# Kernel optimization log

Measured on AMD Instinct MI355X. Metric: run time of the kernel, lower is better.

Reference implementation:

```python
import jax, jax.numpy as jnp
import numpy as np

DIM = 256
NUM_ATOMS = 1024
SPARSITY = 8
BETA = 0.25
EPS = 1e-10


def setup_inputs() -> dict:
    key = jax.random.key(0)
    k1, k2, k3, k4 = jax.random.split(key, 4)
    z_e = jax.random.normal(k1, (32, DIM, 32, 32), dtype=jnp.float32)
    dict_w = jax.random.normal(k2, (NUM_ATOMS, DIM), dtype=jnp.float32)
    rep_w = jax.random.normal(k3, (NUM_ATOMS, DIM), dtype=jnp.float32) * (1.0 / np.sqrt(DIM))
    rep_b = jnp.zeros((NUM_ATOMS,), dtype=jnp.float32)
    return {"z_e": z_e, "dict_w": dict_w, "rep_w": rep_w, "rep_b": rep_b}


def reference(z_e, dict_w, rep_w, rep_b):
    # NCHW -> NHWC, flatten to [N, D]
    ze = jnp.transpose(z_e, (0, 2, 3, 1))
    ze_shape = ze.shape
    flat = ze.reshape(-1, DIM)  # [N, D]
    n = flat.shape[0]

    # representation: Linear + softmax over atoms
    rep = jax.nn.softmax(flat @ rep_w.T + rep_b, axis=1)  # [N, K]

    # squared distances to dictionary atoms
    dists = (jnp.sum(flat ** 2, axis=1, keepdims=True)
             + jnp.sum(dict_w ** 2, axis=1)
             - 2.0 * (flat @ dict_w.T))  # [N, K]

    # top-L smallest distances
    _, idx = jax.lax.top_k(-dists, SPARSITY)  # [N, L]

    # one-hot scatter of selected atoms
    encodings = jnp.zeros((n, NUM_ATOMS), dtype=flat.dtype)
    encodings = encodings.at[jnp.arange(n)[:, None], idx].set(1.0)

    rep_sparse = encodings * rep / SPARSITY  # [N, K]
    z_dl = (rep_sparse @ dict_w).reshape(ze_shape)  # [B, H, W, D]

    e_latent_loss = jnp.mean((jax.lax.stop_gradient(z_dl) - ze) ** 2)
    loss = BETA * e_latent_loss

    # straight-through estimator
    z_st = ze + jax.lax.stop_gradient(z_dl - ze)

    avg_probs = jnp.mean(encodings, axis=0)
    avg_probs = avg_probs / jnp.sum(avg_probs)
    perplexity = jnp.exp(-jnp.sum(avg_probs * jnp.log(avg_probs + EPS)))

    return loss, jnp.transpose(z_st, (0, 3, 1, 2)), perplexity, rep_sparse
```

## Files before the change

kernel.cpp:

```cpp
#include <hip/hip_runtime.h>
#include <hip/hip_bf16.h>
#include <stdint.h>

#define NROWS   32768
#define DIMD    256
#define NATOMS  1024

typedef short  bf16x8 __attribute__((ext_vector_type(8)));
typedef float  f32x4  __attribute__((ext_vector_type(4)));

__device__ __forceinline__ unsigned short bf16rne(float f) {
    unsigned u = __float_as_uint(f);
    u = u + 0x7FFFu + ((u >> 16) & 1u);
    return (unsigned short)(u >> 16);
}

__global__ __launch_bounds__(256) void vq_bprep(
    const float* __restrict__ rep_w, const float* __restrict__ dict_w,
    unsigned short* __restrict__ Bs, float* __restrict__ dnorm,
    int* __restrict__ counts)
{
    const int tid = threadIdx.x;
    if (blockIdx.x == 0) {
        for (int i = tid; i < NATOMS; i += 256) counts[i] = 0;
    }
    const int atom = blockIdx.x * 32 + (tid >> 3);
    const int kc = tid & 7;
    float ss = 0.f;
#pragma unroll
    for (int m = 0; m < 2; ++m) {
        const float* src = (m ? dict_w : rep_w) + (size_t)atom * DIMD + kc * 32;
        unsigned short* dst = Bs + (size_t)m * 262144 + (size_t)kc * 32768 + atom * 32;
#pragma unroll
        for (int q = 0; q < 8; ++q) {
            float4 v = *(const float4*)&src[q * 4];
            float fv[4] = {v.x, v.y, v.z, v.w};
            unsigned short a0[4];
#pragma unroll
            for (int e = 0; e < 4; ++e) {
                if (m) ss = fmaf(fv[e], fv[e], ss);
                a0[e] = bf16rne(fv[e]);
            }
            *(ushort4*)&dst[q * 4] = make_ushort4(a0[0], a0[1], a0[2], a0[3]);
        }
    }
    ss += __shfl_down(ss, 4, 8);
    ss += __shfl_down(ss, 2, 8);
    ss += __shfl_down(ss, 1, 8);
    if (kc == 0) dnorm[atom] = ss;
}

__device__ __forceinline__ void insk(unsigned u, unsigned (&kd)[8]) {
#pragma unroll
    for (int j = 7; j >= 1; --j)
        kd[j] = min(max(u, kd[j - 1]), kd[j]);
    kd[0] = min(u, kd[0]);
}

__device__ __forceinline__ void wave_merge_k(int lane, unsigned (&kd)[8], float& se) {
#pragma unroll
    for (int half = 32; half >= 16; half >>= 1) {
        const int src = (lane + half) & 63;
        unsigned ko[8];
#pragma unroll
        for (int j = 0; j < 8; ++j) ko[j] = (unsigned)__shfl((int)kd[j], src, 64);
        const float so = __shfl(se, src, 64);
        if (lane < half) {
            se += so;
#pragma unroll
            for (int t = 0; t < 8; ++t) insk(ko[t], kd);
        }
    }
}

__global__ __launch_bounds__(256, 3) void vq_main(
    const float* __restrict__ z_e, const unsigned short* __restrict__ Bs,
    const float* __restrict__ rep_b, const float* __restrict__ dnorm,
    int* __restrict__ idx_out, float* __restrict__ fsum_out)
{
    __shared__ __align__(16) float rbS[1024];
    __shared__ __align__(16) float dnS[1024];
    __shared__ unsigned mKu[3][32][8];
    __shared__ float mS[3][32];
    __shared__ unsigned fK[32][8];
    __shared__ float fSum[32];

    const int tid = threadIdx.x;
    const int lane = tid & 63, w = tid >> 6;
    const int c = lane & 15, lg = lane >> 4;
    const int row0 = blockIdx.x * 32;
    const int bb = row0 >> 10, hw0 = row0 & 1023;

    for (int i = tid; i < 1024; i += 256) { rbS[i] = rep_b[i]; dnS[i] = dnorm[i]; }

    const char* pL = (const char*)Bs;
    const char* pD = (const char*)Bs + 524288;
    const int abase = w << 8;

    bf16x8 bL[8], bD[8];
    {
        const int off = ((abase + c) << 6) + (lg << 4);
#pragma unroll
        for (int kc = 0; kc < 8; ++kc) {
            bL[kc] = *(const bf16x8*)(pL + ((size_t)kc << 16) + off);
            bD[kc] = *(const bf16x8*)(pD + ((size_t)kc << 16) + off);
        }
    }

    bf16x8 A0[8], A1[8];
    {
        const float* zb = z_e + (size_t)bb * 262144 + hw0 + c;
#pragma unroll
        for (int kc = 0; kc < 8; ++kc) {
            float f0[8], f1[8];
#pragma unroll
            for (int e = 0; e < 8; ++e) {
                const float* p = zb + (size_t)(kc * 32 + lg * 8 + e) * 1024;
                f0[e] = p[0];
                f1[e] = p[16];
            }
#pragma unroll
            for (int e = 0; e < 8; ++e) {
                A0[kc][e] = (short)bf16rne(f0[e]);
                A1[kc][e] = (short)bf16rne(f1[e]);
            }
        }
    }
    __syncthreads();

    unsigned kd0[8], kd1[8];
    float se0 = 0.f, se1 = 0.f;
#pragma unroll
    for (int j = 0; j < 8; ++j) { kd0[j] = 0xFFFFFFFFu; kd1[j] = 0xFFFFFFFFu; }

    for (int it = 0; it < 16; ++it) {
        const int tb = abase + (it << 4) + (lg << 2);
        const f32x4 rbv = *(const f32x4*)&rbS[tb];
        const f32x4 dnv = *(const f32x4*)&dnS[tb];

        f32x4 aL0 = {0.f,0.f,0.f,0.f}, aD0 = {0.f,0.f,0.f,0.f};
        f32x4 aL1 = {0.f,0.f,0.f,0.f}, aD1 = {0.f,0.f,0.f,0.f};
#pragma unroll
        for (int kc = 0; kc < 8; ++kc) {
            aL0 = __builtin_amdgcn_mfma_f32_16x16x32_bf16(bL[kc], A0[kc], aL0, 0, 0, 0);
            aD0 = __builtin_amdgcn_mfma_f32_16x16x32_bf16(bD[kc], A0[kc], aD0, 0, 0, 0);
            aL1 = __builtin_amdgcn_mfma_f32_16x16x32_bf16(bL[kc], A1[kc], aL1, 0, 0, 0);
            aD1 = __builtin_amdgcn_mfma_f32_16x16x32_bf16(bD[kc], A1[kc], aD1, 0, 0, 0);
        }

        if (it < 15) {
            const int off = ((abase + (it + 1) * 16 + c) << 6) + (lg << 4);
#pragma unroll
            for (int kc = 0; kc < 8; ++kc) {
                bL[kc] = *(const bf16x8*)(pL + ((size_t)kc << 16) + off);
                bD[kc] = *(const bf16x8*)(pD + ((size_t)kc << 16) + off);
            }
        }

#pragma unroll
        for (int q = 0; q < 4; ++q) {
            const unsigned atom = (unsigned)(tb + q);
            se0 += __expf(aL0[q] + rbv[q]);
            se1 += __expf(aL1[q] + rbv[q]);
            unsigned u0 = __float_as_uint(dnv[q] - 2.0f * aD0[q]);
            u0 ^= ((unsigned)((int)u0 >> 31) | 0x80000000u);
            unsigned u1 = __float_as_uint(dnv[q] - 2.0f * aD1[q]);
            u1 ^= ((unsigned)((int)u1 >> 31) | 0x80000000u);
            insk((u0 & ~1023u) | atom, kd0);
            insk((u1 & ~1023u) | atom, kd1);
        }
    }

    wave_merge_k(lane, kd0, se0);
    wave_merge_k(lane, kd1, se1);

    if (w >= 1 && lane < 16) {
#pragma unroll
        for (int j = 0; j < 8; ++j) {
            mKu[w - 1][c][j] = kd0[j];
            mKu[w - 1][16 + c][j] = kd1[j];
        }
        mS[w - 1][c] = se0;
        mS[w - 1][16 + c] = se1;
    }
    __syncthreads();

    if (w == 0 && lane < 16) {
        for (int p = 0; p < 3; ++p)
#pragma unroll
            for (int t = 0; t < 8; ++t) {
                insk(mKu[p][c][t], kd0);
                insk(mKu[p][16 + c][t], kd1);
            }
        se0 += mS[0][c] + mS[1][c] + mS[2][c];
        se1 += mS[0][16 + c] + mS[1][16 + c] + mS[2][16 + c];
#pragma unroll
        for (int j = 0; j < 8; ++j) { fK[c][j] = kd0[j]; fK[16 + c][j] = kd1[j]; }
        fSum[c] = se0;
        fSum[16 + c] = se1;
    }
    __syncthreads();

    {
        const int j = tid >> 5, rr = tid & 31;
        idx_out[(row0 + rr) * 8 + j] = (int)(fK[rr][j] & 1023u);
    }
    if (tid < 32) fsum_out[row0 + tid] = fSum[tid];
}

__global__ __launch_bounds__(256, 4) void vq_recon(
    const float* __restrict__ z_e, const float* __restrict__ dict_w,
    const float* __restrict__ rep_w, const float* __restrict__ rep_b,
    const int* __restrict__ idx_in, const float* __restrict__ fsum_in,
    float* __restrict__ rep_sparse, float* __restrict__ z_st,
    float* __restrict__ partials, int* __restrict__ counts)
{
    __shared__ __align__(16) float zL[32][260];
    __shared__ int   iS[256];
    __shared__ float wS[256];
    __shared__ float fS[32];
    __shared__ float red[256];

    const int tid = threadIdx.x;
    const int row0 = blockIdx.x * 32;
    const int bb = row0 >> 10, hw0 = row0 & 1023;
    const float* zb = z_e + (size_t)bb * 262144 + hw0;

    {
        float4 z4 = {0.f, 0.f, 0.f, 0.f};
        float4* rp4 = (float4*)rep_sparse + (size_t)row0 * (NATOMS / 4) + tid;
        for (int r = 0; r < 32; ++r)
            rp4[(size_t)r * (NATOMS / 4)] = z4;
    }

    iS[tid] = idx_in[row0 * 8 + tid];
    if (tid < 32) fS[tid] = fsum_in[row0 + tid];
    {
        const int m = tid & 31, dg = tid >> 5;
        for (int it = 0; it < 32; ++it) {
            const int d = it * 8 + dg;
            zL[m][d] = zb[(size_t)d * 1024 + m];
        }
    }
    __syncthreads();

    {
        const int j = tid >> 5, rr = tid & 31;
        const int idx = iS[rr * 8 + j];
        const float* rw = rep_w + (size_t)idx * DIMD;
        float acc = 0.f;
        for (int k = 0; k < DIMD; k += 4) {
            const float4 rv = *(const float4*)&rw[k];
            const f32x4 zv = *(const f32x4*)&zL[rr][k];
            acc = fmaf(zv[0], rv.x, acc);
            acc = fmaf(zv[1], rv.y, acc);
            acc = fmaf(zv[2], rv.z, acc);
            acc = fmaf(zv[3], rv.w, acc);
        }
        wS[rr * 8 + j] = __expf(acc + rep_b[idx]) * 0.125f / fS[rr];
    }
    __syncthreads();

    {
        const int j = tid >> 5, rr = tid & 31;
        rep_sparse[(size_t)(row0 + rr) * NATOMS + iS[rr * 8 + j]] = wS[rr * 8 + j];
    }

    float sacc = 0.f;
    for (int r = 0; r < 32; ++r) {
        float acc = 0.f;
#pragma unroll
        for (int j = 0; j < 8; ++j) {
            const int ix = iS[r * 8 + j];
            const float wv = wS[r * 8 + j];
            acc = fmaf(wv, dict_w[(size_t)ix * DIMD + tid], acc);
        }
        const float ze = zL[r][tid];
        const float diff = acc - ze;
        sacc = fmaf(diff, diff, sacc);
        zL[r][tid] = acc;
    }
    __syncthreads();

    {
        float* ob = z_st + (size_t)bb * 262144 + hw0;
        const int m = tid & 31, dg = tid >> 5;
        for (int it = 0; it < 32; ++it) {
            const int d = it * 8 + dg;
            ob[(size_t)d * 1024 + m] = zL[m][d];
        }
    }

    red[tid] = sacc;
    __syncthreads();
    for (int s = 128; s > 0; s >>= 1) {
        if (tid < s) red[tid] += red[tid + s];
        __syncthreads();
    }
    if (tid == 0) partials[blockIdx.x] = red[0];

    __syncthreads();
    int* hS = (int*)zL;
    for (int i = tid; i < 1024; i += 256) hS[i] = 0;
    __syncthreads();
    atomicAdd(&hS[iS[tid]], 1);
    __syncthreads();
    for (int i = tid; i < 1024; i += 256)
        if (hS[i]) atomicAdd(&counts[i], hS[i]);
}

__global__ void vq_final(const float* __restrict__ partials,
                         const int* __restrict__ counts,
                         float* __restrict__ out_loss, float* __restrict__ out_perp)
{
    __shared__ double dred[256];
    __shared__ float fred[256];
    const int tid = threadIdx.x;
    double s = 0.0;
    for (int i = tid; i < 1024; i += 256) s += (double)partials[i];
    dred[tid] = s;
    __syncthreads();
    for (int st = 128; st > 0; st >>= 1) {
        if (tid < st) dred[tid] += dred[tid + st];
        __syncthreads();
    }
    float ps = 0.f;
    for (int i = tid; i < NATOMS; i += 256) {
        const float p = (float)counts[i] * (1.0f / 262144.0f);
        ps += p * logf(p + 1e-10f);
    }
    fred[tid] = ps;
    __syncthreads();
    for (int st = 128; st > 0; st >>= 1) {
        if (tid < st) fred[tid] += fred[tid + st];
        __syncthreads();
    }
    if (tid == 0) {
        *out_loss = 0.25f * (float)(dred[0] / 8388608.0);
        *out_perp = expf(-fred[0]);
    }
}

extern "C" void kernel_launch(void* const* d_in, const int* in_sizes, int n_in,
                              void* d_out, int out_size, void* d_ws, size_t ws_size,
                              hipStream_t stream) {
    const float* z_e    = (const float*)d_in[0];
    const float* dict_w = (const float*)d_in[1];
    const float* rep_w  = (const float*)d_in[2];
    const float* rep_b  = (const float*)d_in[3];

    float* out = (float*)d_out;
    float* out_loss   = out;
    float* z_st       = out + 1;
    float* out_perp   = out + 1 + 8388608;
    float* rep_sparse = out + 2 + 8388608;

    unsigned short* Bs = (unsigned short*)((((uintptr_t)(z_st + 4194304)) + 255) & ~(uintptr_t)255);

    char* ws = (char*)d_ws;
    int*   idx_out  = (int*)ws;
    float* fsum_out = (float*)(ws + (1 << 20));
    int*   counts   = (int*)(ws + (1 << 20) + (1 << 17));
    float* dnorm    = (float*)(ws + (1 << 20) + (1 << 17) + 4096);
    float* partials = (float*)(ws + (1 << 20) + (1 << 17) + 8192);

    vq_bprep<<<32, 256, 0, stream>>>(rep_w, dict_w, Bs, dnorm, counts);
    vq_main<<<NROWS / 32, 256, 0, stream>>>(z_e, Bs, rep_b, dnorm,
                                            idx_out, fsum_out);
    vq_recon<<<NROWS / 32, 256, 0, stream>>>(z_e, dict_w, rep_w, rep_b,
                                             idx_out, fsum_out,
                                             rep_sparse, z_st, partials, counts);
    vq_final<<<1, 256, 0, stream>>>(partials, counts, out_loss, out_perp);
}
```

Baseline: 163.8 us.

## Process 64 rows per block in vq_main to reuse streamed dictionary fragments

```diff
diff --git a/kernel.cpp b/kernel.cpp
--- a/kernel.cpp
+++ b/kernel.cpp
@@ -73,22 +73,22 @@
     }
 }
 
-__global__ __launch_bounds__(256, 3) void vq_main(
+__global__ __launch_bounds__(256, 2) void vq_main(
     const float* __restrict__ z_e, const unsigned short* __restrict__ Bs,
     const float* __restrict__ rep_b, const float* __restrict__ dnorm,
     int* __restrict__ idx_out, float* __restrict__ fsum_out)
 {
     __shared__ __align__(16) float rbS[1024];
     __shared__ __align__(16) float dnS[1024];
-    __shared__ unsigned mKu[3][32][8];
-    __shared__ float mS[3][32];
-    __shared__ unsigned fK[32][8];
-    __shared__ float fSum[32];
+    __shared__ unsigned mKu[3][64][8];
+    __shared__ float mS[3][64];
+    __shared__ unsigned fK[64][8];
+    __shared__ float fSum[64];
 
     const int tid = threadIdx.x;
     const int lane = tid & 63, w = tid >> 6;
     const int c = lane & 15, lg = lane >> 4;
-    const int row0 = blockIdx.x * 32;
+    const int row0 = blockIdx.x * 64;
     const int bb = row0 >> 10, hw0 = row0 & 1023;
 
     for (int i = tid; i < 1024; i += 256) { rbS[i] = rep_b[i]; dnS[i] = dnorm[i]; }
@@ -107,45 +107,58 @@
         }
     }
 
-    bf16x8 A0[8], A1[8];
+    bf16x8 A[4][8];
     {
         const float* zb = z_e + (size_t)bb * 262144 + hw0 + c;
 #pragma unroll
         for (int kc = 0; kc < 8; ++kc) {
-            float f0[8], f1[8];
+            float f[4][8];
 #pragma unroll
             for (int e = 0; e < 8; ++e) {
                 const float* p = zb + (size_t)(kc * 32 + lg * 8 + e) * 1024;
-                f0[e] = p[0];
-                f1[e] = p[16];
-            }
-#pragma unroll
-            for (int e = 0; e < 8; ++e) {
-                A0[kc][e] = (short)bf16rne(f0[e]);
-                A1[kc][e] = (short)bf16rne(f1[e]);
-            }
-        }
-    }
-    __syncthreads();
-
-    unsigned kd0[8], kd1[8];
-    float se0 = 0.f, se1 = 0.f;
-#pragma unroll
-    for (int j = 0; j < 8; ++j) { kd0[j] = 0xFFFFFFFFu; kd1[j] = 0xFFFFFFFFu; }
+                f[0][e] = p[0];
+                f[1][e] = p[16];
+                f[2][e] = p[32];
+                f[3][e] = p[48];
+            }
+#pragma unroll
+            for (int rf = 0; rf < 4; ++rf)
+#pragma unroll
+                for (int e = 0; e < 8; ++e)
+                    A[rf][kc][e] = (short)bf16rne(f[rf][e]);
+        }
+    }
+    __syncthreads();
+
+    unsigned kd[4][8];
+    float se[4] = {0.f, 0.f, 0.f, 0.f};
+#pragma unroll
+    for (int rf = 0; rf < 4; ++rf)
+#pragma unroll
+        for (int j = 0; j < 8; ++j) kd[rf][j] = 0xFFFFFFFFu;
 
     for (int it = 0; it < 16; ++it) {
         const int tb = abase + (it << 4) + (lg << 2);
         const f32x4 rbv = *(const f32x4*)&rbS[tb];
         const f32x4 dnv = *(const f32x4*)&dnS[tb];
 
-        f32x4 aL0 = {0.f,0.f,0.f,0.f}, aD0 = {0.f,0.f,0.f,0.f};
-        f32x4 aL1 = {0.f,0.f,0.f,0.f}, aD1 = {0.f,0.f,0.f,0.f};
-#pragma unroll
-        for (int kc = 0; kc < 8; ++kc) {
-            aL0 = __builtin_amdgcn_mfma_f32_16x16x32_bf16(bL[kc], A0[kc], aL0, 0, 0, 0);
-            aD0 = __builtin_amdgcn_mfma_f32_16x16x32_bf16(bD[kc], A0[kc], aD0, 0, 0, 0);
-            aL1 = __builtin_amdgcn_mfma_f32_16x16x32_bf16(bL[kc], A1[kc], aL1, 0, 0, 0);
-            aD1 = __builtin_amdgcn_mfma_f32_16x16x32_bf16(bD[kc], A1[kc], aD1, 0, 0, 0);
+#pragma unroll
+        for (int rf = 0; rf < 4; ++rf) {
+            f32x4 aL = {0.f, 0.f, 0.f, 0.f};
+            f32x4 aD = {0.f, 0.f, 0.f, 0.f};
+#pragma unroll
+            for (int kc = 0; kc < 8; ++kc) {
+                aL = __builtin_amdgcn_mfma_f32_16x16x32_bf16(bL[kc], A[rf][kc], aL, 0, 0, 0);
+                aD = __builtin_amdgcn_mfma_f32_16x16x32_bf16(bD[kc], A[rf][kc], aD, 0, 0, 0);
+            }
+#pragma unroll
+            for (int q = 0; q < 4; ++q) {
+                const unsigned atom = (unsigned)(tb + q);
+                se[rf] += __expf(aL[q] + rbv[q]);
+                unsigned u = __float_as_uint(dnv[q] - 2.0f * aD[q]);
+                u ^= ((unsigned)((int)u >> 31) | 0x80000000u);
+                insk((u & ~1023u) | atom, kd[rf]);
+            }
         }
 
         if (it < 15) {
@@ -156,56 +169,45 @@
                 bD[kc] = *(const bf16x8*)(pD + ((size_t)kc << 16) + off);
             }
         }
-
-#pragma unroll
-        for (int q = 0; q < 4; ++q) {
-            const unsigned atom = (unsigned)(tb + q);
-            se0 += __expf(aL0[q] + rbv[q]);
-            se1 += __expf(aL1[q] + rbv[q]);
-            unsigned u0 = __float_as_uint(dnv[q] - 2.0f * aD0[q]);
-            u0 ^= ((unsigned)((int)u0 >> 31) | 0x80000000u);
-            unsigned u1 = __float_as_uint(dnv[q] - 2.0f * aD1[q]);
-            u1 ^= ((unsigned)((int)u1 >> 31) | 0x80000000u);
-            insk((u0 & ~1023u) | atom, kd0);
-            insk((u1 & ~1023u) | atom, kd1);
-        }
-    }
-
-    wave_merge_k(lane, kd0, se0);
-    wave_merge_k(lane, kd1, se1);
+    }
+
+#pragma unroll
+    for (int rf = 0; rf < 4; ++rf)
+        wave_merge_k(lane, kd[rf], se[rf]);
 
     if (w >= 1 && lane < 16) {
 #pragma unroll
-        for (int j = 0; j < 8; ++j) {
-            mKu[w - 1][c][j] = kd0[j];
-            mKu[w - 1][16 + c][j] = kd1[j];
-        }
-        mS[w - 1][c] = se0;
-        mS[w - 1][16 + c] = se1;
+        for (int rf = 0; rf < 4; ++rf) {
+#pragma unroll
+            for (int j = 0; j < 8; ++j)
+                mKu[w - 1][rf * 16 + c][j] = kd[rf][j];
+            mS[w - 1][rf * 16 + c] = se[rf];
+        }
     }
     __syncthreads();
 
     if (w == 0 && lane < 16) {
-        for (int p = 0; p < 3; ++p)
-#pragma unroll
-            for (int t = 0; t < 8; ++t) {
-                insk(mKu[p][c][t], kd0);
-                insk(mKu[p][16 + c][t], kd1);
-            }
-        se0 += mS[0][c] + mS[1][c] + mS[2][c];
-        se1 += mS[0][16 + c] + mS[1][16 + c] + mS[2][16 + c];
-#pragma unroll
-        for (int j = 0; j < 8; ++j) { fK[c][j] = kd0[j]; fK[16 + c][j] = kd1[j]; }
-        fSum[c] = se0;
-        fSum[16 + c] = se1;
+#pragma unroll
+        for (int rf = 0; rf < 4; ++rf) {
+            const int rloc = rf * 16 + c;
+            for (int p = 0; p < 3; ++p)
+#pragma unroll
+                for (int t = 0; t < 8; ++t)
+                    insk(mKu[p][rloc][t], kd[rf]);
+            se[rf] += mS[0][rloc] + mS[1][rloc] + mS[2][rloc];
+#pragma unroll
+            for (int j = 0; j < 8; ++j) fK[rloc][j] = kd[rf][j];
+            fSum[rloc] = se[rf];
+        }
     }
     __syncthreads();
 
     {
         const int j = tid >> 5, rr = tid & 31;
-        idx_out[(row0 + rr) * 8 + j] = (int)(fK[rr][j] & 1023u);
-    }
-    if (tid < 32) fsum_out[row0 + tid] = fSum[tid];
+        idx_out[(row0 + rr) * 8 + j]      = (int)(fK[rr][j] & 1023u);
+        idx_out[(row0 + 32 + rr) * 8 + j] = (int)(fK[32 + rr][j] & 1023u);
+    }
+    if (tid < 64) fsum_out[row0 + tid] = fSum[tid];
 }
 
 __global__ __launch_bounds__(256, 4) void vq_recon(
@@ -365,7 +367,7 @@
     float* partials = (float*)(ws + (1 << 20) + (1 << 17) + 8192);
 
     vq_bprep<<<32, 256, 0, stream>>>(rep_w, dict_w, Bs, dnorm, counts);
-    vq_main<<<NROWS / 32, 256, 0, stream>>>(z_e, Bs, rep_b, dnorm,
+    vq_main<<<NROWS / 64, 256, 0, stream>>>(z_e, Bs, rep_b, dnorm,
                                             idx_out, fsum_out);
     vq_recon<<<NROWS / 32, 256, 0, stream>>>(z_e, dict_w, rep_w, rep_b,
                                              idx_out, fsum_out,
```

New measurement: 150.7 us. 8.0% less time.
